# Optimization experiments

Hardware: AMD Instinct MI355X
Metric: run time of the kernel (lower is better)

Reference implementation:

```python
import jax, jax.numpy as jnp
import numpy as np

B, T, D, H, NW = 2, 2048, 1024, 16, 64
HD = D // H  # 64
EPS = 1e-12  # F.normalize eps


def setup_inputs() -> dict:
    key = jax.random.key(0)
    ks = jax.random.split(key, 8)
    def lin(k, din, dout):
        return jax.random.normal(k, (din, dout), jnp.float32) / np.sqrt(din).astype(np.float32)
    return {
        "x": jax.random.normal(ks[0], (B, T, D), jnp.float32),
        "Wqf": lin(ks[1], D, H * NW), "bqf": jnp.zeros((H * NW,), jnp.float32),
        "Wkf": lin(ks[2], D, H * NW), "bkf": jnp.zeros((H * NW,), jnp.float32),
        "Wqp": lin(ks[3], D, H * NW), "bqp": jnp.zeros((H * NW,), jnp.float32),
        "Wkp": lin(ks[4], D, H * NW), "bkp": jnp.zeros((H * NW,), jnp.float32),
        "Wv": lin(ks[5], D, D), "bv": jnp.zeros((D,), jnp.float32),
        "Wo": lin(ks[6], D, D), "bo": jnp.zeros((D,), jnp.float32),
        "scale": jnp.ones((H, 1, 1), jnp.float32),  # interference_scale
    }


def reference(x, Wqf, bqf, Wkf, bkf, Wqp, bqp, Wkp, bkp, Wv, bv, Wo, bo, scale):
    Bx, Tx, Dx = x.shape
    def heads(W, b, nd):  # [B,T,H*nd] -> [B,H,T,nd]
        return jnp.transpose((x @ W + b).reshape(Bx, Tx, H, nd), (0, 2, 1, 3))
    qf = heads(Wqf, bqf, NW); kf = heads(Wkf, bkf, NW)
    qp = heads(Wqp, bqp, NW); kp = heads(Wkp, bkp, NW)
    v = heads(Wv, bv, HD)
    t = jnp.arange(Tx, dtype=x.dtype)[None, None, :, None]  # [1,1,T,1]
    def wave_norm(f, p):
        w = jnp.sin(f * t + p)  # [B,H,T,NW]
        n = jnp.sqrt(jnp.sum(w * w, axis=-1, keepdims=True))
        return w / jnp.maximum(n, EPS)
    qn = wave_norm(qf, qp)
    kn = wave_norm(kf, kp)
    inter = jnp.einsum('bhtw,bhsw->bhts', qn, kn) * scale[None]  # [B,H,T,T]
    causal = jnp.tril(jnp.ones((Tx, Tx), bool))  # keep diag and below
    inter = jnp.where(causal, inter, jnp.zeros((), x.dtype))
    denom = jnp.sqrt(jnp.arange(1, Tx + 1, dtype=x.dtype))[:, None]  # [T,1]
    attn = inter / denom
    # dropout is identity in eval mode
    out = jnp.einsum('bhts,bhsd->bhtd', attn, v)
    out = jnp.transpose(out, (0, 2, 1, 3)).reshape(Bx, Tx, Dx)
    return out @ Wo + bo
```

## Files before the change

### kernel.cpp

```cpp
#include <hip/hip_runtime.h>


#define Bb 2
#define Tt 2048
#define Dd 1024
#define Hh 16
#define NC 32

typedef _Float16 half_t;
typedef _Float16 half8 __attribute__((ext_vector_type(8)));
typedef _Float16 half4h __attribute__((ext_vector_type(4)));
typedef float float4v __attribute__((ext_vector_type(4)));
typedef float f32x16 __attribute__((ext_vector_type(16)));

#define MFMA16(a, b, c) __builtin_amdgcn_mfma_f32_16x16x32_f16((a), (b), (c), 0, 0, 0)
#define MFMA32(a, b, c) __builtin_amdgcn_mfma_f32_32x32x16_f16((a), (b), (c), 0, 0, 0)


#define LOADREGS(K)                                                            \
  rg0 = *(const half8*)&srcHi[(K)];      rg1 = *(const half8*)&srcHi[(K) + 8]; \
  rg2 = *(const half8*)&srcHi[(K) + 16]; rg3 = *(const half8*)&srcHi[(K) + 24];\
  rg4 = *(const half8*)&srcLo[(K)];      rg5 = *(const half8*)&srcLo[(K) + 8]; \
  rg6 = *(const half8*)&srcLo[(K) + 16]; rg7 = *(const half8*)&srcLo[(K) + 24];

#define WRITEFRAGS {                                                           \
  *(half8*)&dHi[0]    = rg0;  *(half8*)&dHi[256]  = rg1;                       \
  *(half8*)&dHi[2048] = rg2;  *(half8*)&dHi[2304] = rg3;                       \
  *(half8*)&dLo[0]    = rg4;  *(half8*)&dLo[256]  = rg5;                       \
  *(half8*)&dLo[2048] = rg6;  *(half8*)&dLo[2304] = rg7; }

#define KTILE_MFMA                                                             \
  _Pragma("unroll")                                                            \
  for (int ks = 0; ks < 2; ++ks) {                                             \
    half8 ahi = *(const half8*)&AhiF[(ks * 4 + w) * 512 + lane * 8];           \
    half8 alo = *(const half8*)&AloF[(ks * 4 + w) * 512 + lane * 8];           \
    _Pragma("unroll")                                                          \
    for (int tn = 0; tn < 4; ++tn) {                                           \
      half8 bhi = *(const half8*)&BhiF[(ks * 4 + tn) * 512 + lane * 8];        \
      half8 blo = *(const half8*)&BloF[(ks * 4 + tn) * 512 + lane * 8];        \
      hh[tn] = MFMA32(ahi, bhi, hh[tn]);                                       \
      mx[tn] = MFMA32(ahi, blo, mx[tn]);                                       \
      mx[tn] = MFMA32(alo, bhi, mx[tn]);                                       \
    }                                                                          \
  }

__global__ __launch_bounds__(256) void xsplit_kernel(
    const float* __restrict__ X, half_t* __restrict__ XHI, half_t* __restrict__ XLO)
{
  const size_t i = ((size_t)blockIdx.x * 256 + threadIdx.x) * 8;
  float4 a = *(const float4*)&X[i];
  float4 b = *(const float4*)&X[i + 4];
  const float av[8] = {a.x, a.y, a.z, a.w, b.x, b.y, b.z, b.w};
  half8 hv, lv;
  #pragma unroll
  for (int j = 0; j < 8; ++j) {
    half_t hx = (half_t)av[j];
    hv[j] = hx; lv[j] = (half_t)((av[j] - (float)hx) * 2048.f);
  }
  *(half8*)&XHI[i] = hv;
  *(half8*)&XLO[i] = lv;
}

__global__ __launch_bounds__(256) void wsplit_kernel(
    const float* __restrict__ W0, const float* __restrict__ W1,
    const float* __restrict__ W2, const float* __restrict__ W3,
    const float* __restrict__ W4, const float* __restrict__ W5,
    half_t* __restrict__ WSP)
{
  __shared__ float Ld[64][68];
  const int tid = threadIdx.x;
  const int m = blockIdx.z;
  const float* W = (m == 0) ? W0 : (m == 1) ? W1 : (m == 2) ? W2
                 : (m == 3) ? W3 : (m == 4) ? W4 : W5;
  const int k0 = blockIdx.x * 64, n0 = blockIdx.y * 64;
  const int r = tid >> 2, c4 = (tid & 3) * 16;
  #pragma unroll
  for (int i = 0; i < 4; ++i)
    *(float4*)&Ld[r][c4 + i * 4] =
        *(const float4*)&W[(size_t)(k0 + r) * Dd + n0 + c4 + i * 4];
  __syncthreads();
  half_t* hi = WSP + (size_t)m * 2097152;
  half_t* lo = hi + 1048576;
  const int n = tid >> 2, kc = (tid & 3) * 16;
  half8 hv0, hv1, lv0, lv1;
  #pragma unroll
  for (int i = 0; i < 8; ++i) {
    float v0 = Ld[kc + i][n];
    half_t h0 = (half_t)v0;
    hv0[i] = h0; lv0[i] = (half_t)((v0 - (float)h0) * 2048.f);
    float v1 = Ld[kc + 8 + i][n];
    half_t h1 = (half_t)v1;
    hv1[i] = h1; lv1[i] = (half_t)((v1 - (float)h1) * 2048.f);
  }
  *(half8*)&hi[(size_t)(n0 + n) * Dd + k0 + kc]     = hv0;
  *(half8*)&hi[(size_t)(n0 + n) * Dd + k0 + kc + 8] = hv1;
  *(half8*)&lo[(size_t)(n0 + n) * Dd + k0 + kc]     = lv0;
  *(half8*)&lo[(size_t)(n0 + n) * Dd + k0 + kc + 8] = lv1;
}

__global__ __launch_bounds__(256, 2) void proj_kernel(
    const half_t* __restrict__ XHI, const half_t* __restrict__ XLO,
    const half_t* __restrict__ WSP,
    const float* __restrict__ bqf, const float* __restrict__ bqp,
    const float* __restrict__ bkf, const float* __restrict__ bkp,
    half_t* __restrict__ QNH, half_t* __restrict__ KNH)
{
  __shared__ __align__(16) half_t AhiF[4096];
  __shared__ __align__(16) half_t AloF[4096];
  __shared__ __align__(16) half_t BhiF[4096];
  __shared__ __align__(16) half_t BloF[4096];
  const int tid = threadIdx.x;
  const int mb = blockIdx.x, h = blockIdx.y;
  const int b = blockIdx.z >> 1, p = blockIdx.z & 1;
  const int t0 = mb * 128, row0 = b * Tt + t0, col0 = h * 64;
  const half_t* WF = WSP + (size_t)(2 * p) * 2097152;
  const half_t* WP = WSP + (size_t)(2 * p + 1) * 2097152;
  const float* BF = p ? bkf : bqf;
  const float* BP = p ? bkp : bqp;
  half_t* OUTH = p ? KNH : QNH;

  f32x16 hh[4], mx[4];
  #pragma unroll
  for (int i = 0; i < 4; ++i) { hh[i] = (f32x16)(0.f); mx[i] = (f32x16)(0.f); }

  const int lane = tid & 63, w = tid >> 6;
  const int rl = lane & 31, kq = lane >> 5;

  const int r = tid & 127, isB = tid >> 7;
  const int rt = r >> 5, rr = r & 31;
  const half_t* srcHi;
  const half_t* srcLo;
  if (!isB) {
    srcHi = &XHI[(size_t)(row0 + r) * Dd];
    srcLo = &XLO[(size_t)(row0 + r) * Dd];
  } else {
    const half_t* Wb = (r < 64) ? (WF + (size_t)(col0 + r) * Dd)
                                : (WP + (size_t)(col0 + r - 64) * Dd);
    srcHi = Wb; srcLo = Wb + 1048576;
  }
  half_t* dHi = (isB ? BhiF : AhiF) + rt * 512 + rr * 8;
  half_t* dLo = (isB ? BloF : AloF) + rt * 512 + rr * 8;

  half8 rg0, rg1, rg2, rg3, rg4, rg5, rg6, rg7;
  LOADREGS(0)

  for (int k0 = 0; k0 < Dd; k0 += 32) {
    WRITEFRAGS
    __syncthreads();
    if (k0 + 32 < Dd) { LOADREGS(k0 + 32) }
    KTILE_MFMA
    __syncthreads();
  }

  const float bf0 = BF[col0 + rl], bf1 = BF[col0 + 32 + rl];
  const float bp0 = BP[col0 + rl], bp1 = BP[col0 + 32 + rl];
  #pragma unroll
  for (int j = 0; j < 16; ++j) {
    const int rtj = (j & 3) + 8 * (j >> 2) + 4 * kq;
    const float tf = (float)(t0 + 32 * w + rtj);
    float f0 = hh[0][j] + mx[0][j] * (1.f / 2048.f) + bf0;
    float f1 = hh[1][j] + mx[1][j] * (1.f / 2048.f) + bf1;
    float p0 = hh[2][j] + mx[2][j] * (1.f / 2048.f) + bp0;
    float p1 = hh[3][j] + mx[3][j] * (1.f / 2048.f) + bp1;
    float w0 = sinf(fmaf(f0, tf, p0));
    float w1 = sinf(fmaf(f1, tf, p1));
    float ss = w0 * w0 + w1 * w1;
    ss += __shfl_xor(ss, 1); ss += __shfl_xor(ss, 2);
    ss += __shfl_xor(ss, 4); ss += __shfl_xor(ss, 8);
    ss += __shfl_xor(ss, 16);
    const float inv = 1.f / fmaxf(sqrtf(ss), 1e-12f);
    half_t* op = &OUTH[((size_t)(b * Tt) + t0 + 32 * w + rtj) * Dd + col0];
    op[rl]      = (half_t)(w0 * inv);
    op[32 + rl] = (half_t)(w1 * inv);
  }
}

__global__ __launch_bounds__(256, 2) void gemm_kernel(
    const half_t* __restrict__ AHI, const half_t* __restrict__ ALO,
    const half_t* __restrict__ WHI,
    const float* __restrict__ BIAS, float* __restrict__ OUT)
{
  __shared__ __align__(16) half_t AhiF[4096];
  __shared__ __align__(16) half_t AloF[4096];
  __shared__ __align__(16) half_t BhiF[4096];
  __shared__ __align__(16) half_t BloF[4096];
  const int tid = threadIdx.x;
  const int m0 = blockIdx.x * 128, n0 = blockIdx.y * 128;

  f32x16 hh[4], mx[4];
  #pragma unroll
  for (int i = 0; i < 4; ++i) { hh[i] = (f32x16)(0.f); mx[i] = (f32x16)(0.f); }

  const int lane = tid & 63, w = tid >> 6;
  const int rl = lane & 31, kq = lane >> 5;

  const int r = tid & 127, isB = tid >> 7;
  const int rt = r >> 5, rr = r & 31;
  const half_t* srcHi = isB ? &WHI[(size_t)(n0 + r) * Dd]
                            : &AHI[(size_t)(m0 + r) * Dd];
  const half_t* srcLo = isB ? &WHI[1048576 + (size_t)(n0 + r) * Dd]
                            : &ALO[(size_t)(m0 + r) * Dd];
  half_t* dHi = (isB ? BhiF : AhiF) + rt * 512 + rr * 8;
  half_t* dLo = (isB ? BloF : AloF) + rt * 512 + rr * 8;

  half8 rg0, rg1, rg2, rg3, rg4, rg5, rg6, rg7;
  LOADREGS(0)

  for (int k0 = 0; k0 < Dd; k0 += 32) {
    WRITEFRAGS
    __syncthreads();
    if (k0 + 32 < Dd) { LOADREGS(k0 + 32) }
    KTILE_MFMA
    __syncthreads();
  }

  const float bb0 = BIAS[n0 + rl],      bb1 = BIAS[n0 + 32 + rl];
  const float bb2 = BIAS[n0 + 64 + rl], bb3 = BIAS[n0 + 96 + rl];
  #pragma unroll
  for (int j = 0; j < 16; ++j) {
    const int rtj = (j & 3) + 8 * (j >> 2) + 4 * kq;
    float* orow = &OUT[(size_t)(m0 + 32 * w + rtj) * Dd + n0];
    orow[rl]      = hh[0][j] + mx[0][j] * (1.f / 2048.f) + bb0;
    orow[32 + rl] = hh[1][j] + mx[1][j] * (1.f / 2048.f) + bb1;
    orow[64 + rl] = hh[2][j] + mx[2][j] * (1.f / 2048.f) + bb2;
    orow[96 + rl] = hh[3][j] + mx[3][j] * (1.f / 2048.f) + bb3;
  }
}

__global__ __launch_bounds__(256) void chunk_kv_kernel(
    const half_t* __restrict__ KNH, const float* __restrict__ V,
    float* __restrict__ G)
{
  __shared__ float Ks[64][64];
  __shared__ float Vs[64][64];
  const int tid = threadIdx.x;
  const int c = blockIdx.x, h = blockIdx.y, b = blockIdx.z;
  const int s0 = c * 64;
  const int lr = tid >> 2, lc = (tid & 3) * 16;
  {
    const half_t* krow = &KNH[(size_t)(b * Tt + s0 + lr) * Dd + h * 64 + lc];
    half8 ka = *(const half8*)&krow[0];
    half8 kb = *(const half8*)&krow[8];
    #pragma unroll
    for (int i = 0; i < 8; ++i) {
      Ks[lr][lc + i] = (float)ka[i];
      Ks[lr][lc + 8 + i] = (float)kb[i];
    }
    const float* vrow = &V[(size_t)(b * Tt + s0 + lr) * Dd + h * 64 + lc];
    #pragma unroll
    for (int i = 0; i < 4; ++i)
      *(float4*)&Vs[lr][lc + i * 4] = *(const float4*)&vrow[i * 4];
  }
  __syncthreads();

  const int ty = tid >> 4, tx = tid & 15;
  float g[4][4] = {{0.f}};
  #pragma unroll 4
  for (int s = 0; s < 64; ++s) {
    float4 kv = *(const float4*)&Ks[s][ty * 4];
    float4 vv = *(const float4*)&Vs[s][tx * 4];
    const float* k_ = (const float*)&kv;
    const float* v_ = (const float*)&vv;
    #pragma unroll
    for (int i = 0; i < 4; ++i)
      #pragma unroll
      for (int j = 0; j < 4; ++j)
        g[i][j] = fmaf(k_[i], v_[j], g[i][j]);
  }
  float* Gp = G + (((size_t)(b * Hh + h) * NC + c) << 12);
  #pragma unroll
  for (int i = 0; i < 4; ++i)
    *(float4*)&Gp[(ty * 4 + i) * 64 + tx * 4] =
        make_float4(g[i][0], g[i][1], g[i][2], g[i][3]);
}

__global__ __launch_bounds__(256) void prefix_kernel(float* __restrict__ G)
{
  const int seg = blockIdx.x, h = blockIdx.y, b = blockIdx.z;
  float* base = G + (((size_t)(b * Hh + h) * NC) << 12) + seg * 256 + threadIdx.x;
  float acc = 0.f;
  #pragma unroll 4
  for (int c = 0; c < NC; ++c) {
    float* p = base + ((size_t)c << 12);
    const float g = *p;
    *p = acc;
    acc += g;
  }
}

__global__ __launch_bounds__(256) void attn_chunk_kernel(
    const half_t* __restrict__ QNH, const half_t* __restrict__ KNH,
    const float* __restrict__ V, const float* __restrict__ M,
    const float* __restrict__ SCALE,
    half_t* __restrict__ ATTHI, half_t* __restrict__ ATTLO)
{
  __shared__ float Qt[64][68];
  __shared__ float Kt[64][68];
  __shared__ float SM[64][68];
  __shared__ float Vs[64][64];
  const int tid = threadIdx.x;
  const int c = blockIdx.x, h = blockIdx.y, b = blockIdx.z;
  const int t0 = c * 64;
  const int lr = tid >> 2, lc = (tid & 3) * 16;
  {
    const half_t* qrow = &QNH[(size_t)(b * Tt + t0 + lr) * Dd + h * 64 + lc];
    const half_t* krow = &KNH[(size_t)(b * Tt + t0 + lr) * Dd + h * 64 + lc];
    half8 qa = *(const half8*)&qrow[0];
    half8 qb = *(const half8*)&qrow[8];
    half8 ka = *(const half8*)&krow[0];
    half8 kb = *(const half8*)&krow[8];
    #pragma unroll
    for (int i = 0; i < 8; ++i) {
      Qt[lc + i][lr] = (float)qa[i];     Qt[lc + 8 + i][lr] = (float)qb[i];
      Kt[lc + i][lr] = (float)ka[i];     Kt[lc + 8 + i][lr] = (float)kb[i];
    }
    const float* vrow = &V[(size_t)(b * Tt + t0 + lr) * Dd + h * 64 + lc];
    const float* mrow = &M[(((size_t)(b * Hh + h) * NC + c) << 12) + lr * 64 + lc];
    #pragma unroll
    for (int i = 0; i < 4; ++i) {
      *(float4*)&Vs[lr][lc + i * 4] = *(const float4*)&vrow[i * 4];
      *(float4*)&SM[lr][lc + i * 4] = *(const float4*)&mrow[i * 4];
    }
  }
  __syncthreads();

  const int ty = tid >> 4, tx = tid & 15;
  float o[4][4] = {{0.f}};
  float sc[4][4] = {{0.f}};

  #pragma unroll 4
  for (int w = 0; w < 64; ++w) {
    float4 qv = *(const float4*)&Qt[w][ty * 4];
    float4 mv = *(const float4*)&SM[w][tx * 4];
    float4 kv = *(const float4*)&Kt[w][tx * 4];
    const float* q_ = (const float*)&qv;
    const float* m_ = (const float*)&mv;
    const float* k_ = (const float*)&kv;
    #pragma unroll
    for (int i = 0; i < 4; ++i) {
      float qq = q_[i];
      #pragma unroll
      for (int j = 0; j < 4; ++j) {
        o[i][j]  = fmaf(qq, m_[j], o[i][j]);
        sc[i][j] = fmaf(qq, k_[j], sc[i][j]);
      }
    }
  }
  __syncthreads();

  #pragma unroll
  for (int i = 0; i < 4; ++i) {
    const int lt = ty * 4 + i;
    #pragma unroll
    for (int j = 0; j < 4; ++j) {
      const int ls = tx * 4 + j;
      SM[ls][lt] = (ls <= lt) ? sc[i][j] : 0.f;
    }
  }
  __syncthreads();

  #pragma unroll 4
  for (int s = 0; s < 64; ++s) {
    float4 sv = *(const float4*)&SM[s][ty * 4];
    float4 vv = *(const float4*)&Vs[s][tx * 4];
    const float* s_ = (const float*)&sv;
    const float* v_ = (const float*)&vv;
    #pragma unroll
    for (int i = 0; i < 4; ++i)
      #pragma unroll
      for (int j = 0; j < 4; ++j)
        o[i][j] = fmaf(s_[i], v_[j], o[i][j]);
  }

  const float sch = SCALE[h];
  #pragma unroll
  for (int i = 0; i < 4; ++i) {
    const int t = t0 + ty * 4 + i;
    const float fac = sch / sqrtf((float)(t + 1));
    half4h hv, lv;
    #pragma unroll
    for (int j = 0; j < 4; ++j) {
      float v = o[i][j] * fac;
      half_t hx = (half_t)v;
      hv[j] = hx; lv[j] = (half_t)((v - (float)hx) * 2048.f);
    }
    *(half4h*)&ATTHI[(size_t)(b * Tt + t) * Dd + h * 64 + tx * 4] = hv;
    *(half4h*)&ATTLO[(size_t)(b * Tt + t) * Dd + h * 64 + tx * 4] = lv;
  }
}

extern "C" void kernel_launch(void* const* d_in, const int* in_sizes, int n_in,
                              void* d_out, int out_size, void* d_ws, size_t ws_size,
                              hipStream_t stream) {
  const float* x   = (const float*)d_in[0];
  const float* Wqf = (const float*)d_in[1];
  const float* bqf = (const float*)d_in[2];
  const float* Wkf = (const float*)d_in[3];
  const float* bkf = (const float*)d_in[4];
  const float* Wqp = (const float*)d_in[5];
  const float* bqp = (const float*)d_in[6];
  const float* Wkp = (const float*)d_in[7];
  const float* bkp = (const float*)d_in[8];
  const float* Wv  = (const float*)d_in[9];
  const float* bv  = (const float*)d_in[10];
  const float* Wo  = (const float*)d_in[11];
  const float* bo  = (const float*)d_in[12];
  const float* scale = (const float*)d_in[13];

  half_t* WSP = (half_t*)d_ws;
  half_t* qnh = WSP + 12582912;
  half_t* knh = qnh + 4194304;
  float*  G   = (float*)(knh + 4194304);
  half_t* xhi = (half_t*)G;
  half_t* xlo = xhi + 4194304;
  float*  vbuf = (float*)d_out;

  xsplit_kernel<<<dim3(2048), 256, 0, stream>>>(x, xhi, xlo);

  wsplit_kernel<<<dim3(16, 16, 6), 256, 0, stream>>>(Wqf, Wqp, Wkf, Wkp, Wv, Wo, WSP);

  proj_kernel<<<dim3(Tt / 128, Hh, Bb * 2), 256, 0, stream>>>(
      xhi, xlo, WSP, bqf, bqp, bkf, bkp, qnh, knh);

  gemm_kernel<<<dim3((Bb * Tt) / 128, Dd / 128), 256, 0, stream>>>(
      xhi, xlo, WSP + (size_t)4 * 2097152, bv, vbuf);

  chunk_kv_kernel<<<dim3(NC, Hh, Bb), 256, 0, stream>>>(knh, vbuf, G);
  prefix_kernel<<<dim3(16, Hh, Bb), 256, 0, stream>>>(G);
  attn_chunk_kernel<<<dim3(NC, Hh, Bb), 256, 0, stream>>>(
      qnh, knh, vbuf, G, scale, qnh , knh );

  gemm_kernel<<<dim3((Bb * Tt) / 128, Dd / 128), 256, 0, stream>>>(
      qnh, knh, WSP + (size_t)5 * 2097152, bo, (float*)d_out);
}
```

Baseline: 400.4 us.

## Use XOR-swizzled LDS tiles, 2x2 warp tiling and double buffering in GEMMs

Replaces the fragment-ordered LDS layout with row-major tiles whose 16-byte chunks are XOR-swizzled, to avoid bank conflicts, in both the projection and output GEMM kernels. The output GEMM also moves from a 4x1 to a 2x2 wave layout, which cuts the B-operand LDS reads per wave, and double-buffers the LDS tiles so each k-step needs one barrier instead of two. This doubles that kernel's shared memory, which may lower occupancy under the launch bound of 2 blocks.

```diff
diff --git a/kernel.cpp b/kernel.cpp
--- a/kernel.cpp
+++ b/kernel.cpp
@@ -16,33 +16,11 @@
 #define MFMA16(a, b, c) __builtin_amdgcn_mfma_f32_16x16x32_f16((a), (b), (c), 0, 0, 0)
 #define MFMA32(a, b, c) __builtin_amdgcn_mfma_f32_32x32x16_f16((a), (b), (c), 0, 0, 0)
 
-
 #define LOADREGS(K)                                                            \
   rg0 = *(const half8*)&srcHi[(K)];      rg1 = *(const half8*)&srcHi[(K) + 8]; \
   rg2 = *(const half8*)&srcHi[(K) + 16]; rg3 = *(const half8*)&srcHi[(K) + 24];\
   rg4 = *(const half8*)&srcLo[(K)];      rg5 = *(const half8*)&srcLo[(K) + 8]; \
   rg6 = *(const half8*)&srcLo[(K) + 16]; rg7 = *(const half8*)&srcLo[(K) + 24];
-
-#define WRITEFRAGS {                                                           \
-  *(half8*)&dHi[0]    = rg0;  *(half8*)&dHi[256]  = rg1;                       \
-  *(half8*)&dHi[2048] = rg2;  *(half8*)&dHi[2304] = rg3;                       \
-  *(half8*)&dLo[0]    = rg4;  *(half8*)&dLo[256]  = rg5;                       \
-  *(half8*)&dLo[2048] = rg6;  *(half8*)&dLo[2304] = rg7; }
-
-#define KTILE_MFMA                                                             \
-  _Pragma("unroll")                                                            \
-  for (int ks = 0; ks < 2; ++ks) {                                             \
-    half8 ahi = *(const half8*)&AhiF[(ks * 4 + w) * 512 + lane * 8];           \
-    half8 alo = *(const half8*)&AloF[(ks * 4 + w) * 512 + lane * 8];           \
-    _Pragma("unroll")                                                          \
-    for (int tn = 0; tn < 4; ++tn) {                                           \
-      half8 bhi = *(const half8*)&BhiF[(ks * 4 + tn) * 512 + lane * 8];        \
-      half8 blo = *(const half8*)&BloF[(ks * 4 + tn) * 512 + lane * 8];        \
-      hh[tn] = MFMA32(ahi, bhi, hh[tn]);                                       \
-      mx[tn] = MFMA32(ahi, blo, mx[tn]);                                       \
-      mx[tn] = MFMA32(alo, bhi, mx[tn]);                                       \
-    }                                                                          \
-  }
 
 __global__ __launch_bounds__(256) void xsplit_kernel(
     const float* __restrict__ X, half_t* __restrict__ XHI, half_t* __restrict__ XLO)
@@ -105,10 +83,8 @@
     const float* __restrict__ bkf, const float* __restrict__ bkp,
     half_t* __restrict__ QNH, half_t* __restrict__ KNH)
 {
-  __shared__ __align__(16) half_t AhiF[4096];
-  __shared__ __align__(16) half_t AloF[4096];
-  __shared__ __align__(16) half_t BhiF[4096];
-  __shared__ __align__(16) half_t BloF[4096];
+  __shared__ __align__(16) half_t As[128][64];
+  __shared__ __align__(16) half_t Bs[128][64];
   const int tid = threadIdx.x;
   const int mb = blockIdx.x, h = blockIdx.y;
   const int b = blockIdx.z >> 1, p = blockIdx.z & 1;
@@ -125,9 +101,10 @@
 
   const int lane = tid & 63, w = tid >> 6;
   const int rl = lane & 31, kq = lane >> 5;
+  const int sw = rl & 7;
 
   const int r = tid & 127, isB = tid >> 7;
-  const int rt = r >> 5, rr = r & 31;
+  const int swr = r & 7;
   const half_t* srcHi;
   const half_t* srcLo;
   if (!isB) {
@@ -138,17 +115,35 @@
                                 : (WP + (size_t)(col0 + r - 64) * Dd);
     srcHi = Wb; srcLo = Wb + 1048576;
   }
-  half_t* dHi = (isB ? BhiF : AhiF) + rt * 512 + rr * 8;
-  half_t* dLo = (isB ? BloF : AloF) + rt * 512 + rr * 8;
+  half_t* dstRow = isB ? &Bs[r][0] : &As[r][0];
+  const int pc0 = (0 ^ swr) * 8, pc1 = (1 ^ swr) * 8;
+  const int pc2 = (2 ^ swr) * 8, pc3 = (3 ^ swr) * 8;
+  const int pc4 = (4 ^ swr) * 8, pc5 = (5 ^ swr) * 8;
+  const int pc6 = (6 ^ swr) * 8, pc7 = (7 ^ swr) * 8;
 
   half8 rg0, rg1, rg2, rg3, rg4, rg5, rg6, rg7;
   LOADREGS(0)
 
   for (int k0 = 0; k0 < Dd; k0 += 32) {
-    WRITEFRAGS
+    *(half8*)&dstRow[pc0] = rg0; *(half8*)&dstRow[pc1] = rg1;
+    *(half8*)&dstRow[pc2] = rg2; *(half8*)&dstRow[pc3] = rg3;
+    *(half8*)&dstRow[pc4] = rg4; *(half8*)&dstRow[pc5] = rg5;
+    *(half8*)&dstRow[pc6] = rg6; *(half8*)&dstRow[pc7] = rg7;
     __syncthreads();
     if (k0 + 32 < Dd) { LOADREGS(k0 + 32) }
-    KTILE_MFMA
+    #pragma unroll
+    for (int ks = 0; ks < 2; ++ks) {
+      half8 ahi = *(const half8*)&As[32 * w + rl][((2 * ks + kq) ^ sw) * 8];
+      half8 alo = *(const half8*)&As[32 * w + rl][((4 + 2 * ks + kq) ^ sw) * 8];
+      #pragma unroll
+      for (int tn = 0; tn < 4; ++tn) {
+        half8 bhi = *(const half8*)&Bs[32 * tn + rl][((2 * ks + kq) ^ sw) * 8];
+        half8 blo = *(const half8*)&Bs[32 * tn + rl][((4 + 2 * ks + kq) ^ sw) * 8];
+        hh[tn] = MFMA32(ahi, bhi, hh[tn]);
+        mx[tn] = MFMA32(ahi, blo, mx[tn]);
+        mx[tn] = MFMA32(alo, bhi, mx[tn]);
+      }
+    }
     __syncthreads();
   }
 
@@ -180,10 +175,8 @@
     const half_t* __restrict__ WHI,
     const float* __restrict__ BIAS, float* __restrict__ OUT)
 {
-  __shared__ __align__(16) half_t AhiF[4096];
-  __shared__ __align__(16) half_t AloF[4096];
-  __shared__ __align__(16) half_t BhiF[4096];
-  __shared__ __align__(16) half_t BloF[4096];
+  __shared__ __align__(16) half_t As[2][128][64];
+  __shared__ __align__(16) half_t Bs[2][128][64];
   const int tid = threadIdx.x;
   const int m0 = blockIdx.x * 128, n0 = blockIdx.y * 128;
 
@@ -193,38 +186,84 @@
 
   const int lane = tid & 63, w = tid >> 6;
   const int rl = lane & 31, kq = lane >> 5;
+  const int sw = rl & 7;
+  const int wm = w >> 1, wn = w & 1;
 
   const int r = tid & 127, isB = tid >> 7;
-  const int rt = r >> 5, rr = r & 31;
+  const int swr = r & 7;
   const half_t* srcHi = isB ? &WHI[(size_t)(n0 + r) * Dd]
                             : &AHI[(size_t)(m0 + r) * Dd];
   const half_t* srcLo = isB ? &WHI[1048576 + (size_t)(n0 + r) * Dd]
                             : &ALO[(size_t)(m0 + r) * Dd];
-  half_t* dHi = (isB ? BhiF : AhiF) + rt * 512 + rr * 8;
-  half_t* dLo = (isB ? BloF : AloF) + rt * 512 + rr * 8;
+  half_t* dstRow = isB ? &Bs[0][r][0] : &As[0][r][0];
+  const int pc0 = (0 ^ swr) * 8, pc1 = (1 ^ swr) * 8;
+  const int pc2 = (2 ^ swr) * 8, pc3 = (3 ^ swr) * 8;
+  const int pc4 = (4 ^ swr) * 8, pc5 = (5 ^ swr) * 8;
+  const int pc6 = (6 ^ swr) * 8, pc7 = (7 ^ swr) * 8;
 
   half8 rg0, rg1, rg2, rg3, rg4, rg5, rg6, rg7;
+
+#define WRITE_G(BI) {                                                      \
+    half_t* d_ = dstRow + (BI) * 8192;                                     \
+    *(half8*)&d_[pc0] = rg0; *(half8*)&d_[pc1] = rg1;                      \
+    *(half8*)&d_[pc2] = rg2; *(half8*)&d_[pc3] = rg3;                      \
+    *(half8*)&d_[pc4] = rg4; *(half8*)&d_[pc5] = rg5;                      \
+    *(half8*)&d_[pc6] = rg6; *(half8*)&d_[pc7] = rg7; }
+
+#define KTILE_G(BI)                                                        \
+  _Pragma("unroll")                                                        \
+  for (int ks = 0; ks < 2; ++ks) {                                         \
+    const int ch = ((2 * ks + kq) ^ sw) * 8;                               \
+    const int cl = ((4 + 2 * ks + kq) ^ sw) * 8;                           \
+    half8 a0h = *(const half8*)&As[BI][64 * wm + rl][ch];                  \
+    half8 a0l = *(const half8*)&As[BI][64 * wm + rl][cl];                  \
+    half8 a1h = *(const half8*)&As[BI][64 * wm + 32 + rl][ch];             \
+    half8 a1l = *(const half8*)&As[BI][64 * wm + 32 + rl][cl];             \
+    half8 b0h = *(const half8*)&Bs[BI][64 * wn + rl][ch];                  \
+    half8 b0l = *(const half8*)&Bs[BI][64 * wn + rl][cl];                  \
+    half8 b1h = *(const half8*)&Bs[BI][64 * wn + 32 + rl][ch];             \
+    half8 b1l = *(const half8*)&Bs[BI][64 * wn + 32 + rl][cl];             \
+    hh[0] = MFMA32(a0h, b0h, hh[0]);                                       \
+    mx[0] = MFMA32(a0h, b0l, mx[0]); mx[0] = MFMA32(a0l, b0h, mx[0]);      \
+    hh[1] = MFMA32(a0h, b1h, hh[1]);                                       \
+    mx[1] = MFMA32(a0h, b1l, mx[1]); mx[1] = MFMA32(a0l, b1h, mx[1]);      \
+    hh[2] = MFMA32(a1h, b0h, hh[2]);                                       \
+    mx[2] = MFMA32(a1h, b0l, mx[2]); mx[2] = MFMA32(a1l, b0h, mx[2]);      \
+    hh[3] = MFMA32(a1h, b1h, hh[3]);                                       \
+    mx[3] = MFMA32(a1h, b1l, mx[3]); mx[3] = MFMA32(a1l, b1h, mx[3]);      \
+  }
+
   LOADREGS(0)
-
-  for (int k0 = 0; k0 < Dd; k0 += 32) {
-    WRITEFRAGS
+  WRITE_G(0)
+  LOADREGS(32)
+  __syncthreads();
+
+  #pragma unroll 1
+  for (int k0 = 0; k0 < Dd; k0 += 64) {
+    KTILE_G(0)
+    WRITE_G(1)
+    if (k0 + 64 < Dd) { LOADREGS(k0 + 64) }
     __syncthreads();
-    if (k0 + 32 < Dd) { LOADREGS(k0 + 32) }
-    KTILE_MFMA
+    KTILE_G(1)
+    if (k0 + 64 < Dd) { WRITE_G(0) }
+    if (k0 + 96 < Dd) { LOADREGS(k0 + 96) }
     __syncthreads();
   }
 
-  const float bb0 = BIAS[n0 + rl],      bb1 = BIAS[n0 + 32 + rl];
-  const float bb2 = BIAS[n0 + 64 + rl], bb3 = BIAS[n0 + 96 + rl];
+  const float bb0 = BIAS[n0 + 64 * wn + rl];
+  const float bb1 = BIAS[n0 + 64 * wn + 32 + rl];
   #pragma unroll
   for (int j = 0; j < 16; ++j) {
     const int rtj = (j & 3) + 8 * (j >> 2) + 4 * kq;
-    float* orow = &OUT[(size_t)(m0 + 32 * w + rtj) * Dd + n0];
-    orow[rl]      = hh[0][j] + mx[0][j] * (1.f / 2048.f) + bb0;
-    orow[32 + rl] = hh[1][j] + mx[1][j] * (1.f / 2048.f) + bb1;
-    orow[64 + rl] = hh[2][j] + mx[2][j] * (1.f / 2048.f) + bb2;
-    orow[96 + rl] = hh[3][j] + mx[3][j] * (1.f / 2048.f) + bb3;
-  }
+    float* or0 = &OUT[(size_t)(m0 + 64 * wm + rtj) * Dd + n0 + 64 * wn];
+    float* or1 = &OUT[(size_t)(m0 + 64 * wm + 32 + rtj) * Dd + n0 + 64 * wn];
+    or0[rl]      = hh[0][j] + mx[0][j] * (1.f / 2048.f) + bb0;
+    or0[32 + rl] = hh[1][j] + mx[1][j] * (1.f / 2048.f) + bb1;
+    or1[rl]      = hh[2][j] + mx[2][j] * (1.f / 2048.f) + bb0;
+    or1[32 + rl] = hh[3][j] + mx[3][j] * (1.f / 2048.f) + bb1;
+  }
+#undef WRITE_G
+#undef KTILE_G
 }
 
 __global__ __launch_bounds__(256) void chunk_kv_kernel(
```

New measurement: 399.6 us. About the same (-0.2%).

## Stage B tiles via global_load_lds double buffer, load A straight to registers

Applied to the files above, without the earlier changes.

Rewrites the projection and GEMM main loops. The weight (B) tiles are now staged into an XOR-swizzled, double-buffered LDS buffer with direct global-to-LDS loads. The activation (A) fragments are loaded from global memory straight into registers in MFMA layout, which removes the A tiles from LDS and drops the register round trip for B. The GEMM tile shrinks to 64x128 with a 2x2 wave layout, doubling the grid. The trade-off is uncoalesced per-lane A loads from global memory and more blocks re-reading the B tiles.

```diff
diff --git a/kernel.cpp b/kernel.cpp
--- a/kernel.cpp
+++ b/kernel.cpp
@@ -10,39 +10,14 @@
 typedef _Float16 half_t;
 typedef _Float16 half8 __attribute__((ext_vector_type(8)));
 typedef _Float16 half4h __attribute__((ext_vector_type(4)));
-typedef float float4v __attribute__((ext_vector_type(4)));
 typedef float f32x16 __attribute__((ext_vector_type(16)));
 
-#define MFMA16(a, b, c) __builtin_amdgcn_mfma_f32_16x16x32_f16((a), (b), (c), 0, 0, 0)
 #define MFMA32(a, b, c) __builtin_amdgcn_mfma_f32_32x32x16_f16((a), (b), (c), 0, 0, 0)
 
-
-#define LOADREGS(K)                                                            \
-  rg0 = *(const half8*)&srcHi[(K)];      rg1 = *(const half8*)&srcHi[(K) + 8]; \
-  rg2 = *(const half8*)&srcHi[(K) + 16]; rg3 = *(const half8*)&srcHi[(K) + 24];\
-  rg4 = *(const half8*)&srcLo[(K)];      rg5 = *(const half8*)&srcLo[(K) + 8]; \
-  rg6 = *(const half8*)&srcLo[(K) + 16]; rg7 = *(const half8*)&srcLo[(K) + 24];
-
-#define WRITEFRAGS {                                                           \
-  *(half8*)&dHi[0]    = rg0;  *(half8*)&dHi[256]  = rg1;                       \
-  *(half8*)&dHi[2048] = rg2;  *(half8*)&dHi[2304] = rg3;                       \
-  *(half8*)&dLo[0]    = rg4;  *(half8*)&dLo[256]  = rg5;                       \
-  *(half8*)&dLo[2048] = rg6;  *(half8*)&dLo[2304] = rg7; }
-
-#define KTILE_MFMA                                                             \
-  _Pragma("unroll")                                                            \
-  for (int ks = 0; ks < 2; ++ks) {                                             \
-    half8 ahi = *(const half8*)&AhiF[(ks * 4 + w) * 512 + lane * 8];           \
-    half8 alo = *(const half8*)&AloF[(ks * 4 + w) * 512 + lane * 8];           \
-    _Pragma("unroll")                                                          \
-    for (int tn = 0; tn < 4; ++tn) {                                           \
-      half8 bhi = *(const half8*)&BhiF[(ks * 4 + tn) * 512 + lane * 8];        \
-      half8 blo = *(const half8*)&BloF[(ks * 4 + tn) * 512 + lane * 8];        \
-      hh[tn] = MFMA32(ahi, bhi, hh[tn]);                                       \
-      mx[tn] = MFMA32(ahi, blo, mx[tn]);                                       \
-      mx[tn] = MFMA32(alo, bhi, mx[tn]);                                       \
-    }                                                                          \
-  }
+#define GLL(G, L) __builtin_amdgcn_global_load_lds(                      \
+    (const __attribute__((address_space(1))) void*)(G),                  \
+    (__attribute__((address_space(3))) void*)(L), 16, 0, 0)
+
 
 __global__ __launch_bounds__(256) void xsplit_kernel(
     const float* __restrict__ X, half_t* __restrict__ XHI, half_t* __restrict__ XLO)
@@ -105,10 +80,7 @@
     const float* __restrict__ bkf, const float* __restrict__ bkp,
     half_t* __restrict__ QNH, half_t* __restrict__ KNH)
 {
-  __shared__ __align__(16) half_t AhiF[4096];
-  __shared__ __align__(16) half_t AloF[4096];
-  __shared__ __align__(16) half_t BhiF[4096];
-  __shared__ __align__(16) half_t BloF[4096];
+  __shared__ __align__(16) half_t Bs[2][128][64];
   const int tid = threadIdx.x;
   const int mb = blockIdx.x, h = blockIdx.y;
   const int b = blockIdx.z >> 1, p = blockIdx.z & 1;
@@ -125,32 +97,67 @@
 
   const int lane = tid & 63, w = tid >> 6;
   const int rl = lane & 31, kq = lane >> 5;
-
-  const int r = tid & 127, isB = tid >> 7;
-  const int rt = r >> 5, rr = r & 31;
-  const half_t* srcHi;
-  const half_t* srcLo;
-  if (!isB) {
-    srcHi = &XHI[(size_t)(row0 + r) * Dd];
-    srcLo = &XLO[(size_t)(row0 + r) * Dd];
-  } else {
-    const half_t* Wb = (r < 64) ? (WF + (size_t)(col0 + r) * Dd)
-                                : (WP + (size_t)(col0 + r - 64) * Dd);
-    srcHi = Wb; srcLo = Wb + 1048576;
-  }
-  half_t* dHi = (isB ? BhiF : AhiF) + rt * 512 + rr * 8;
-  half_t* dLo = (isB ? BloF : AloF) + rt * 512 + rr * 8;
-
-  half8 rg0, rg1, rg2, rg3, rg4, rg5, rg6, rg7;
-  LOADREGS(0)
-
-  for (int k0 = 0; k0 < Dd; k0 += 32) {
-    WRITEFRAGS
+  const int sw = rl & 7;
+
+  const half_t* aHi = XHI + (size_t)(row0 + 32 * w + rl) * Dd + kq * 8;
+  const half_t* aLo = XLO + (size_t)(row0 + 32 * w + rl) * Dd + kq * 8;
+
+  const int lr8 = lane >> 3;
+  const int lcc = (lane & 7) ^ lr8;
+  const int csel = (lcc & 3) * 8;
+  const size_t loOff = (lcc >= 4) ? 1048576 : 0;
+  const half_t* gb0 = WF + loOff + (size_t)(col0 + 8 * w + lr8) * Dd + csel;
+  const half_t* gb1 = gb0 + 32 * Dd;
+  const half_t* gb2 = WP + loOff + (size_t)(col0 + 8 * w + lr8) * Dd + csel;
+  const half_t* gb3 = gb2 + 32 * Dd;
+
+#define STAGE_PB(BI, K) {                          \
+    GLL(gb0 + (K), &Bs[BI][8 * w][0]);             \
+    GLL(gb1 + (K), &Bs[BI][32 + 8 * w][0]);        \
+    GLL(gb2 + (K), &Bs[BI][64 + 8 * w][0]);        \
+    GLL(gb3 + (K), &Bs[BI][96 + 8 * w][0]); }
+
+#define LOADA(H0, H1, L0, L1, K) {                 \
+    H0 = *(const half8*)&aHi[(K)];                 \
+    H1 = *(const half8*)&aHi[(K) + 16];            \
+    L0 = *(const half8*)&aLo[(K)];                 \
+    L1 = *(const half8*)&aLo[(K) + 16]; }
+
+#define KT_P(H0, H1, L0, L1, BI) {                                     \
+    { const int c0 = (kq ^ sw) * 8, c1 = ((4 + kq) ^ sw) * 8;          \
+      _Pragma("unroll")                                                \
+      for (int tn = 0; tn < 4; ++tn) {                                 \
+        half8 bh = *(const half8*)&Bs[BI][32 * tn + rl][c0];           \
+        half8 bl = *(const half8*)&Bs[BI][32 * tn + rl][c1];           \
+        hh[tn] = MFMA32(H0, bh, hh[tn]);                               \
+        mx[tn] = MFMA32(H0, bl, mx[tn]);                               \
+        mx[tn] = MFMA32(L0, bh, mx[tn]); } }                           \
+    { const int c0 = (((2 + kq)) ^ sw) * 8, c1 = ((6 + kq) ^ sw) * 8;  \
+      _Pragma("unroll")                                                \
+      for (int tn = 0; tn < 4; ++tn) {                                 \
+        half8 bh = *(const half8*)&Bs[BI][32 * tn + rl][c0];           \
+        half8 bl = *(const half8*)&Bs[BI][32 * tn + rl][c1];           \
+        hh[tn] = MFMA32(H1, bh, hh[tn]);                               \
+        mx[tn] = MFMA32(H1, bl, mx[tn]);                               \
+        mx[tn] = MFMA32(L1, bh, mx[tn]); } } }
+
+  half8 ah0c, ah1c, al0c, al1c, ah0n, ah1n, al0n, al1n;
+  STAGE_PB(0, 0)
+  LOADA(ah0c, ah1c, al0c, al1c, 0)
+  __syncthreads();
+
+  #pragma unroll 1
+  for (int k0 = 0; k0 < Dd; k0 += 64) {
+    if (k0 + 32 < Dd) { STAGE_PB(1, k0 + 32) LOADA(ah0n, ah1n, al0n, al1n, k0 + 32) }
+    KT_P(ah0c, ah1c, al0c, al1c, 0)
     __syncthreads();
-    if (k0 + 32 < Dd) { LOADREGS(k0 + 32) }
-    KTILE_MFMA
+    if (k0 + 64 < Dd) { STAGE_PB(0, k0 + 64) LOADA(ah0c, ah1c, al0c, al1c, k0 + 64) }
+    KT_P(ah0n, ah1n, al0n, al1n, 1)
     __syncthreads();
   }
+#undef STAGE_PB
+#undef LOADA
+#undef KT_P
 
   const float bf0 = BF[col0 + rl], bf1 = BF[col0 + 32 + rl];
   const float bp0 = BP[col0 + rl], bp1 = BP[col0 + 32 + rl];
@@ -180,50 +187,89 @@
     const half_t* __restrict__ WHI,
     const float* __restrict__ BIAS, float* __restrict__ OUT)
 {
-  __shared__ __align__(16) half_t AhiF[4096];
-  __shared__ __align__(16) half_t AloF[4096];
-  __shared__ __align__(16) half_t BhiF[4096];
-  __shared__ __align__(16) half_t BloF[4096];
+  __shared__ __align__(16) half_t Bs[2][128][64];
   const int tid = threadIdx.x;
-  const int m0 = blockIdx.x * 128, n0 = blockIdx.y * 128;
-
-  f32x16 hh[4], mx[4];
-  #pragma unroll
-  for (int i = 0; i < 4; ++i) { hh[i] = (f32x16)(0.f); mx[i] = (f32x16)(0.f); }
+  const int m0 = blockIdx.x * 64, n0 = blockIdx.y * 128;
+
+  f32x16 hh0 = (f32x16)(0.f), hh1 = (f32x16)(0.f);
+  f32x16 mx0 = (f32x16)(0.f), mx1 = (f32x16)(0.f);
 
   const int lane = tid & 63, w = tid >> 6;
   const int rl = lane & 31, kq = lane >> 5;
-
-  const int r = tid & 127, isB = tid >> 7;
-  const int rt = r >> 5, rr = r & 31;
-  const half_t* srcHi = isB ? &WHI[(size_t)(n0 + r) * Dd]
-                            : &AHI[(size_t)(m0 + r) * Dd];
-  const half_t* srcLo = isB ? &WHI[1048576 + (size_t)(n0 + r) * Dd]
-                            : &ALO[(size_t)(m0 + r) * Dd];
-  half_t* dHi = (isB ? BhiF : AhiF) + rt * 512 + rr * 8;
-  half_t* dLo = (isB ? BloF : AloF) + rt * 512 + rr * 8;
-
-  half8 rg0, rg1, rg2, rg3, rg4, rg5, rg6, rg7;
-  LOADREGS(0)
-
-  for (int k0 = 0; k0 < Dd; k0 += 32) {
-    WRITEFRAGS
+  const int sw = rl & 7;
+  const int wm = w & 1, wn = w >> 1;
+
+  const half_t* aHi = AHI + (size_t)(m0 + 32 * wm + rl) * Dd + kq * 8;
+  const half_t* aLo = ALO + (size_t)(m0 + 32 * wm + rl) * Dd + kq * 8;
+
+  const int lr8 = lane >> 3;
+  const int lcc = (lane & 7) ^ lr8;
+  const int csel = (lcc & 3) * 8;
+  const size_t loOff = (lcc >= 4) ? 1048576 : 0;
+  const half_t* gb0 = WHI + loOff + (size_t)(n0 + 8 * w + lr8) * Dd + csel;
+  const half_t* gb1 = gb0 + 32 * Dd;
+  const half_t* gb2 = gb0 + 64 * Dd;
+  const half_t* gb3 = gb0 + 96 * Dd;
+
+#define STAGE_GB(BI, K) {                          \
+    GLL(gb0 + (K), &Bs[BI][8 * w][0]);             \
+    GLL(gb1 + (K), &Bs[BI][32 + 8 * w][0]);        \
+    GLL(gb2 + (K), &Bs[BI][64 + 8 * w][0]);        \
+    GLL(gb3 + (K), &Bs[BI][96 + 8 * w][0]); }
+
+#define LOADA(H0, H1, L0, L1, K) {                 \
+    H0 = *(const half8*)&aHi[(K)];                 \
+    H1 = *(const half8*)&aHi[(K) + 16];            \
+    L0 = *(const half8*)&aLo[(K)];                 \
+    L1 = *(const half8*)&aLo[(K) + 16]; }
+
+#define KT_G(H0, H1, L0, L1, BI) {                                     \
+    { const int c0 = (kq ^ sw) * 8, c1 = ((4 + kq) ^ sw) * 8;          \
+      half8 bh0 = *(const half8*)&Bs[BI][64 * wn + rl][c0];            \
+      half8 bl0 = *(const half8*)&Bs[BI][64 * wn + rl][c1];            \
+      half8 bh1 = *(const half8*)&Bs[BI][64 * wn + 32 + rl][c0];       \
+      half8 bl1 = *(const half8*)&Bs[BI][64 * wn + 32 + rl][c1];       \
+      hh0 = MFMA32(H0, bh0, hh0); mx0 = MFMA32(H0, bl0, mx0);          \
+      mx0 = MFMA32(L0, bh0, mx0);                                      \
+      hh1 = MFMA32(H0, bh1, hh1); mx1 = MFMA32(H0, bl1, mx1);          \
+      mx1 = MFMA32(L0, bh1, mx1); }                                    \
+    { const int c0 = ((2 + kq) ^ sw) * 8, c1 = ((6 + kq) ^ sw) * 8;    \
+      half8 bh0 = *(const half8*)&Bs[BI][64 * wn + rl][c0];            \
+      half8 bl0 = *(const half8*)&Bs[BI][64 * wn + rl][c1];            \
+      half8 bh1 = *(const half8*)&Bs[BI][64 * wn + 32 + rl][c0];       \
+      half8 bl1 = *(const half8*)&Bs[BI][64 * wn + 32 + rl][c1];       \
+      hh0 = MFMA32(H1, bh0, hh0); mx0 = MFMA32(H1, bl0, mx0);          \
+      mx0 = MFMA32(L1, bh0, mx0);                                      \
+      hh1 = MFMA32(H1, bh1, hh1); mx1 = MFMA32(H1, bl1, mx1);          \
+      mx1 = MFMA32(L1, bh1, mx1); } }
+
+  half8 ah0c, ah1c, al0c, al1c, ah0n, ah1n, al0n, al1n;
+  STAGE_GB(0, 0)
+  LOADA(ah0c, ah1c, al0c, al1c, 0)
+  __syncthreads();
+
+  #pragma unroll 1
+  for (int k0 = 0; k0 < Dd; k0 += 64) {
+    if (k0 + 32 < Dd) { STAGE_GB(1, k0 + 32) LOADA(ah0n, ah1n, al0n, al1n, k0 + 32) }
+    KT_G(ah0c, ah1c, al0c, al1c, 0)
     __syncthreads();
-    if (k0 + 32 < Dd) { LOADREGS(k0 + 32) }
-    KTILE_MFMA
+    if (k0 + 64 < Dd) { STAGE_GB(0, k0 + 64) LOADA(ah0c, ah1c, al0c, al1c, k0 + 64) }
+    KT_G(ah0n, ah1n, al0n, al1n, 1)
     __syncthreads();
   }
-
-  const float bb0 = BIAS[n0 + rl],      bb1 = BIAS[n0 + 32 + rl];
-  const float bb2 = BIAS[n0 + 64 + rl], bb3 = BIAS[n0 + 96 + rl];
+#undef STAGE_GB
+#undef LOADA
+#undef KT_G
+
+  const int colb = n0 + 64 * wn;
+  const float bb0 = BIAS[colb + rl];
+  const float bb1 = BIAS[colb + 32 + rl];
   #pragma unroll
   for (int j = 0; j < 16; ++j) {
     const int rtj = (j & 3) + 8 * (j >> 2) + 4 * kq;
-    float* orow = &OUT[(size_t)(m0 + 32 * w + rtj) * Dd + n0];
-    orow[rl]      = hh[0][j] + mx[0][j] * (1.f / 2048.f) + bb0;
-    orow[32 + rl] = hh[1][j] + mx[1][j] * (1.f / 2048.f) + bb1;
-    orow[64 + rl] = hh[2][j] + mx[2][j] * (1.f / 2048.f) + bb2;
-    orow[96 + rl] = hh[3][j] + mx[3][j] * (1.f / 2048.f) + bb3;
+    float* orow = &OUT[(size_t)(m0 + 32 * wm + rtj) * Dd + colb];
+    orow[rl]      = hh0[j] + mx0[j] * (1.f / 2048.f) + bb0;
+    orow[32 + rl] = hh1[j] + mx1[j] * (1.f / 2048.f) + bb1;
   }
 }
 
@@ -422,7 +468,7 @@
   proj_kernel<<<dim3(Tt / 128, Hh, Bb * 2), 256, 0, stream>>>(
       xhi, xlo, WSP, bqf, bqp, bkf, bkp, qnh, knh);
 
-  gemm_kernel<<<dim3((Bb * Tt) / 128, Dd / 128), 256, 0, stream>>>(
+  gemm_kernel<<<dim3((Bb * Tt) / 64, Dd / 128), 256, 0, stream>>>(
       xhi, xlo, WSP + (size_t)4 * 2097152, bv, vbuf);
 
   chunk_kv_kernel<<<dim3(NC, Hh, Bb), 256, 0, stream>>>(knh, vbuf, G);
@@ -430,6 +476,6 @@
   attn_chunk_kernel<<<dim3(NC, Hh, Bb), 256, 0, stream>>>(
       qnh, knh, vbuf, G, scale, qnh , knh );
 
-  gemm_kernel<<<dim3((Bb * Tt) / 128, Dd / 128), 256, 0, stream>>>(
+  gemm_kernel<<<dim3((Bb * Tt) / 64, Dd / 128), 256, 0, stream>>>(
       qnh, knh, WSP + (size_t)5 * 2097152, bo, (float*)d_out);
 }
```

After: 387.6 us. -3.2%, faster.
